# Kernel optimization log

Hardware: AMD Instinct MI355X
Metric: run time of the kernel (lower is better)

The kernel has to match this reference:

```python
import jax, jax.numpy as jnp
import numpy as np

B, S, H, NH = 4, 2048, 2048, 16
HD = H // NH
EPS = 1e-5


def setup_inputs() -> dict:
    key = jax.random.key(0)
    ks = jax.random.split(key, 5)
    return {
        "x": jax.random.normal(ks[0], (B, S, H), dtype=jnp.float32),
        "ln_w": jnp.ones((H,), dtype=jnp.float32),
        "ln_b": jnp.zeros((H,), dtype=jnp.float32),
        "c_attn_w": jax.random.normal(ks[1], (H, 3 * H), dtype=jnp.float32) * 0.02,
        "c_attn_b": jax.random.normal(ks[2], (3 * H,), dtype=jnp.float32) * 0.02,
        "c_proj_w": jax.random.normal(ks[3], (H, H), dtype=jnp.float32) * 0.02,
        "c_proj_b": jax.random.normal(ks[4], (H,), dtype=jnp.float32) * 0.02,
    }


def reference(x, ln_w, ln_b, c_attn_w, c_attn_b, c_proj_w, c_proj_b):
    residual = x
    # fused layer norm
    mu = jnp.mean(x, axis=-1, keepdims=True)
    var = jnp.mean(jnp.square(x - mu), axis=-1, keepdims=True)
    xn = (x - mu) * jax.lax.rsqrt(var + EPS) * ln_w + ln_b
    qkv = jnp.einsum("bsh,hk->bsk", xn, c_attn_w) + c_attn_b
    q, k, v = jnp.split(qkv, 3, axis=-1)
    def heads(t):
        return t.reshape(B, S, NH, HD).transpose(0, 2, 1, 3)
    q, k, v = heads(q), heads(k), heads(v)
    # causal flash attention (reference math)
    scale = 1.0 / np.sqrt(HD)
    scores = jnp.einsum("bnqd,bnkd->bnqk", q, k) * scale
    causal = jnp.tril(jnp.ones((S, S), dtype=bool))
    scores = jnp.where(causal, scores, jnp.finfo(scores.dtype).min)
    attn = jax.nn.softmax(scores, axis=-1)
    o = jnp.einsum("bnqk,bnkd->bnqd", attn, v)
    # merge heads: [B,NH,S,HD] -> [B,S,H]
    o = o.transpose(0, 2, 1, 3).reshape(B, S, H)
    # output projection + residual (fused_ffn, add_gelu=False, dropout=0)
    return jnp.einsum("bsh,hk->bsk", o, c_proj_w) + c_proj_b + residual
```

## Files before the change

kernel.cpp:

```cpp
#include <hip/hip_runtime.h>
#include <stdint.h>
#include <math.h>

#define B_  4
#define S_  2048
#define H_  2048
#define NH_ 16
#define HD_ 128
#define M_  (B_*S_)
#define N3_ (3*H_)
#define NQT_ (S_/64)
#define NT_ (H_/64)

typedef __attribute__((ext_vector_type(8))) short short8;
typedef __attribute__((ext_vector_type(4))) float floatx4;
typedef unsigned int u32;

__device__ __forceinline__ unsigned short f2bf(float f) {
  unsigned u = __float_as_uint(f);
  u += 0x7FFF + ((u >> 16) & 1);
  return (unsigned short)(u >> 16);
}

__device__ __forceinline__ void gl2lds16(const void* g, void* l) {
  __builtin_amdgcn_global_load_lds(
      (const __attribute__((address_space(1))) u32*)g,
      (__attribute__((address_space(3))) u32*)l, 16, 0, 0);
}

__global__ __launch_bounds__(256) void ln_kernel(
    const float* __restrict__ x, const float* __restrict__ w,
    const float* __restrict__ b, unsigned short* __restrict__ xn) {
  int row = blockIdx.x;
  int t = threadIdx.x;
  const float* xr = x + (size_t)row * H_;
  float4 v0 = *(const float4*)(xr + t * 4);
  float4 v1 = *(const float4*)(xr + 1024 + t * 4);
  float s  = v0.x + v0.y + v0.z + v0.w + v1.x + v1.y + v1.z + v1.w;
  float sq = v0.x*v0.x + v0.y*v0.y + v0.z*v0.z + v0.w*v0.w
           + v1.x*v1.x + v1.y*v1.y + v1.z*v1.z + v1.w*v1.w;
  #pragma unroll
  for (int m = 32; m; m >>= 1) { s += __shfl_xor(s, m); sq += __shfl_xor(sq, m); }
  __shared__ float red[8];
  int wv = t >> 6;
  if ((t & 63) == 0) { red[wv * 2] = s; red[wv * 2 + 1] = sq; }
  __syncthreads();
  s  = red[0] + red[2] + red[4] + red[6];
  sq = red[1] + red[3] + red[5] + red[7];
  float mu  = s * (1.0f / H_);
  float var = sq * (1.0f / H_) - mu * mu;
  float rs  = rsqrtf(var + 1e-5f);

  float4 w0 = *(const float4*)(w + t * 4);
  float4 b0 = *(const float4*)(b + t * 4);
  float4 w1 = *(const float4*)(w + 1024 + t * 4);
  float4 b1 = *(const float4*)(b + 1024 + t * 4);
  ushort4 o0, o1;
  o0.x = f2bf((v0.x - mu) * rs * w0.x + b0.x);
  o0.y = f2bf((v0.y - mu) * rs * w0.y + b0.y);
  o0.z = f2bf((v0.z - mu) * rs * w0.z + b0.z);
  o0.w = f2bf((v0.w - mu) * rs * w0.w + b0.w);
  o1.x = f2bf((v1.x - mu) * rs * w1.x + b1.x);
  o1.y = f2bf((v1.y - mu) * rs * w1.y + b1.y);
  o1.z = f2bf((v1.z - mu) * rs * w1.z + b1.z);
  o1.w = f2bf((v1.w - mu) * rs * w1.w + b1.w);
  unsigned short* orow = xn + (size_t)row * H_;
  *(ushort4*)(orow + t * 4) = o0;
  *(ushort4*)(orow + 1024 + t * 4) = o1;
}

__global__ __launch_bounds__(256) void transpose_f2b(
    const float* __restrict__ in, unsigned short* __restrict__ out,
    int R, int C) {
  __shared__ float tile[32][33];
  int tx = threadIdx.x & 31, ty = threadIdx.x >> 5;
  int c0 = blockIdx.x * 32, r0 = blockIdx.y * 32;
  #pragma unroll
  for (int i = 0; i < 32; i += 8)
    tile[ty + i][tx] = in[(size_t)(r0 + ty + i) * C + c0 + tx];
  __syncthreads();
  #pragma unroll
  for (int i = 0; i < 32; i += 8)
    out[(size_t)(c0 + ty + i) * R + r0 + tx] = f2bf(tile[tx][ty + i]);
}

__device__ __forceinline__ void gemm256_acc(
    const unsigned short* __restrict__ A, const unsigned short* __restrict__ Bt,
    int m0, int n0, unsigned short (*sh)[16384], floatx4 (&acc)[8][4]) {
  const int t = threadIdx.x;
  const int lane = t & 63, wv = t >> 6;
  const int l15 = lane & 15, quad = lane >> 4;
  const int wm = wv >> 2, wn = wv & 3;
  const int x7 = l15 & 7;

  const int aRB = (wm * 128 + l15) * 64;
  const int bRB = (wn * 64 + l15) * 64;
  const int kx0 = ((0 + quad) ^ x7) * 8;
  const int kx1 = ((4 + quad) ^ x7) * 8;

  const int r = t >> 3, cc = t & 7;
  const int scol = (cc ^ (r & 7)) * 8;
  const unsigned short* aSrc = A + (size_t)(m0 + r) * H_ + scol;
  const int btr = (r >> 5) * 64 + (r & 31);
  const unsigned short* bSrc = Bt + (size_t)(n0 + btr) * H_ + scol;
  const int aDst = t * 8;
  const int bDst = (r >> 5) * 4096 + (r & 31) * 64 + cc * 8;

  auto stageAll = [&](int kt, int buf) {
    const unsigned short* sa = aSrc + kt * 64;
    const unsigned short* sb = bSrc + kt * 64;
    unsigned short* da = sh[buf * 2] + aDst;
    unsigned short* db = sh[buf * 2 + 1] + bDst;
    gl2lds16(sa, da);
    gl2lds16(sa + (size_t)128 * H_, da + 8192);
    gl2lds16(sa + (size_t)64 * H_, da + 4096);
    gl2lds16(sa + (size_t)192 * H_, da + 12288);
    gl2lds16(sb, db);
    gl2lds16(sb + (size_t)128 * H_, db + 8192);
    gl2lds16(sb + (size_t)32 * H_, db + 2048);
    gl2lds16(sb + (size_t)160 * H_, db + 10240);
  };

  short8 aE[4][2], aO[4][2], b01[2][2], b23[2][2];
  auto readAE = [&](const unsigned short* Ab) {
    #pragma unroll
    for (int i = 0; i < 4; ++i) {
      aE[i][0] = *(const short8*)(Ab + aRB + i * 1024 + kx0);
      aE[i][1] = *(const short8*)(Ab + aRB + i * 1024 + kx1);
    }
  };
  auto readAO = [&](const unsigned short* Ab) {
    #pragma unroll
    for (int i = 0; i < 4; ++i) {
      aO[i][0] = *(const short8*)(Ab + aRB + (i + 4) * 1024 + kx0);
      aO[i][1] = *(const short8*)(Ab + aRB + (i + 4) * 1024 + kx1);
    }
  };
  auto readB01 = [&](const unsigned short* Bb) {
    #pragma unroll
    for (int j = 0; j < 2; ++j) {
      b01[j][0] = *(const short8*)(Bb + bRB + j * 1024 + kx0);
      b01[j][1] = *(const short8*)(Bb + bRB + j * 1024 + kx1);
    }
  };
  auto readB23 = [&](const unsigned short* Bb) {
    #pragma unroll
    for (int j = 0; j < 2; ++j) {
      b23[j][0] = *(const short8*)(Bb + bRB + (j + 2) * 1024 + kx0);
      b23[j][1] = *(const short8*)(Bb + bRB + (j + 2) * 1024 + kx1);
    }
  };

  #pragma unroll
  for (int i = 0; i < 8; i++)
    #pragma unroll
    for (int j = 0; j < 4; j++) acc[i][j] = (floatx4){0.f, 0.f, 0.f, 0.f};

  stageAll(0, 0);
  stageAll(1, 1);
  asm volatile("s_waitcnt vmcnt(8)" ::: "memory");
  __builtin_amdgcn_s_barrier();
  readAE(sh[0]); readB01(sh[1]);

  for (int n = 0; n < NT_; ++n) {
    const int buf = n & 1;
    const unsigned short* Ab = sh[buf * 2];
    const unsigned short* Bb = sh[buf * 2 + 1];

    readB23(Bb);
    asm volatile("s_waitcnt lgkmcnt(4)" ::: "memory");
    __builtin_amdgcn_sched_barrier(0);
    __builtin_amdgcn_s_setprio(1);
    #pragma unroll
    for (int i = 0; i < 4; ++i)
      #pragma unroll
      for (int j = 0; j < 2; ++j) {
        acc[i][j] = __builtin_amdgcn_mfma_f32_16x16x32_bf16(aE[i][0], b01[j][0], acc[i][j], 0, 0, 0);
        acc[i][j] = __builtin_amdgcn_mfma_f32_16x16x32_bf16(aE[i][1], b01[j][1], acc[i][j], 0, 0, 0);
      }
    __builtin_amdgcn_s_setprio(0);

    readAO(Ab);
    asm volatile("s_waitcnt lgkmcnt(8)" ::: "memory");
    __builtin_amdgcn_sched_barrier(0);
    __builtin_amdgcn_s_setprio(1);
    #pragma unroll
    for (int i = 0; i < 4; ++i)
      #pragma unroll
      for (int j = 0; j < 2; ++j) {
        acc[i][j + 2] = __builtin_amdgcn_mfma_f32_16x16x32_bf16(aE[i][0], b23[j][0], acc[i][j + 2], 0, 0, 0);
        acc[i][j + 2] = __builtin_amdgcn_mfma_f32_16x16x32_bf16(aE[i][1], b23[j][1], acc[i][j + 2], 0, 0, 0);
      }
    __builtin_amdgcn_s_setprio(0);

    asm volatile("s_waitcnt lgkmcnt(0)" ::: "memory");
    __builtin_amdgcn_sched_barrier(0);
    __builtin_amdgcn_s_setprio(1);
    #pragma unroll
    for (int i = 0; i < 4; ++i)
      #pragma unroll
      for (int j = 0; j < 2; ++j) {
        acc[i + 4][j] = __builtin_amdgcn_mfma_f32_16x16x32_bf16(aO[i][0], b01[j][0], acc[i + 4][j], 0, 0, 0);
        acc[i + 4][j] = __builtin_amdgcn_mfma_f32_16x16x32_bf16(aO[i][1], b01[j][1], acc[i + 4][j], 0, 0, 0);
      }
    __builtin_amdgcn_s_setprio(0);

    asm volatile("s_waitcnt vmcnt(0)" ::: "memory");
    __builtin_amdgcn_s_barrier();
    if (n + 1 < NT_) { readAE(sh[(buf ^ 1) * 2]); readB01(sh[(buf ^ 1) * 2 + 1]); }
    if (n + 2 < NT_) stageAll(n + 2, buf);

    __builtin_amdgcn_s_setprio(1);
    #pragma unroll
    for (int i = 0; i < 4; ++i)
      #pragma unroll
      for (int j = 0; j < 2; ++j) {
        acc[i + 4][j + 2] = __builtin_amdgcn_mfma_f32_16x16x32_bf16(aO[i][0], b23[j][0], acc[i + 4][j + 2], 0, 0, 0);
        acc[i + 4][j + 2] = __builtin_amdgcn_mfma_f32_16x16x32_bf16(aO[i][1], b23[j][1], acc[i + 4][j + 2], 0, 0, 0);
      }
    __builtin_amdgcn_s_setprio(0);
  }
}

__device__ __forceinline__ void xcd_map(int& m0, int& n0) {
  int bid = blockIdx.y * gridDim.x + blockIdx.x;
  int xcd = bid & 7, loc = bid >> 3;
  m0 = ((xcd << 2) | (loc & 3)) * 256;
  n0 = (loc >> 2) * 256;
}

__global__ __launch_bounds__(512, 2) void qkv_gemm(
    const unsigned short* __restrict__ A, const unsigned short* __restrict__ Bt,
    const float* __restrict__ bias,
    unsigned short* __restrict__ qw, unsigned short* __restrict__ kw,
    unsigned short* __restrict__ vtw) {
  __shared__ unsigned short sh[4][16384];
  int m0, n0;
  xcd_map(m0, n0);

  floatx4 acc[8][4];
  gemm256_acc(A, Bt, m0, n0, sh, acc);

  int t = threadIdx.x, lane = t & 63, wv = t >> 6;
  int l15 = lane & 15, quad = lane >> 4;
  int wm = wv >> 2, wn = wv & 3;
  int sec = n0 >> 11;
  #pragma unroll
  for (int j = 0; j < 4; ++j) {
    int nn = n0 + wn * 64 + j * 16 + l15;
    int h = (nn >> 7) & 15;
    int d = nn & 127;
    float bval = bias[nn];
    #pragma unroll
    for (int i = 0; i < 8; ++i) {
      int m = m0 + wm * 128 + i * 16 + quad * 4;
      int bb = m >> 11, s = m & 2047;
      int bh = bb * NH_ + h;
      if (sec == 2) {
        ushort4 pv;
        pv.x = f2bf(acc[i][j][0] + bval); pv.y = f2bf(acc[i][j][1] + bval);
        pv.z = f2bf(acc[i][j][2] + bval); pv.w = f2bf(acc[i][j][3] + bval);
        *(ushort4*)(vtw + ((size_t)bh * HD_ + d) * S_ + s) = pv;
      } else {
        unsigned short* dst = (sec == 0 ? qw : kw) + ((size_t)bh * S_ + s) * HD_ + d;
        #pragma unroll
        for (int reg = 0; reg < 4; reg++)
          dst[(size_t)reg * HD_] = f2bf(acc[i][j][reg] + bval);
      }
    }
  }
}

__global__ __launch_bounds__(512, 2) void proj_gemm(
    const unsigned short* __restrict__ A, const unsigned short* __restrict__ Bt,
    const float* __restrict__ bias, const float* __restrict__ resid,
    float* __restrict__ out) {
  __shared__ unsigned short sh[4][16384];
  int m0, n0;
  xcd_map(m0, n0);

  floatx4 acc[8][4];
  gemm256_acc(A, Bt, m0, n0, sh, acc);

  int t = threadIdx.x, lane = t & 63, wv = t >> 6;
  int l15 = lane & 15, quad = lane >> 4;
  int wm = wv >> 2, wn = wv & 3;
  #pragma unroll
  for (int j = 0; j < 4; ++j) {
    int nn = n0 + wn * 64 + j * 16 + l15;
    float bval = bias[nn];
    #pragma unroll
    for (int i = 0; i < 8; ++i) {
      int m = m0 + wm * 128 + i * 16 + quad * 4;
      #pragma unroll
      for (int reg = 0; reg < 4; ++reg)
        out[(size_t)(m + reg) * H_ + nn] =
            acc[i][j][reg] + bval + resid[(size_t)(m + reg) * H_ + nn];
    }
  }
}

__global__ __launch_bounds__(256) void attn_kernel(
    const unsigned short* __restrict__ qw, const unsigned short* __restrict__ kw,
    const unsigned short* __restrict__ vtw, unsigned short* __restrict__ ow) {
  __shared__ unsigned short Klds[64 * 136];
  __shared__ unsigned short Vtl[128 * 72];
  __shared__ unsigned short Pl[4][16 * 72];
  int pr = blockIdx.x, bh = blockIdx.y;
  int t = threadIdx.x, lane = t & 63, wv = t >> 6;
  int l15 = lane & 15, quad = lane >> 4;
  int h = bh & 15, bb = bh >> 4;

  const float scale = 0.08838834764831845f;
  int krr = t >> 4, kcc = (t & 15) * 8;
  int vdd = t >> 3, vss = (t & 7) * 8;
  unsigned short* plw = &Pl[wv][0];
  const unsigned short* kgb = kw + ((size_t)bh * S_ + krr) * HD_ + kcc;
  const unsigned short* vgb = vtw + ((size_t)bh * HD_ + vdd) * S_ + vss;

  short8 kreg[4], vreg[4];
  auto load_stage = [&](int kb) {
    #pragma unroll
    for (int c = 0; c < 4; c++) {
      kreg[c] = *(const short8*)(kgb + (size_t)(kb + c * 16) * HD_);
      vreg[c] = *(const short8*)(vgb + (size_t)(c * 32) * S_ + kb);
    }
  };

  #pragma unroll 1
  for (int half = 0; half < 2; half++) {
    int qt = half ? (NQT_ - 1 - pr) : pr;
    int qr = qt * 64 + wv * 16;
    int q = qr + l15;

    short8 qf[4];
    {
      const unsigned short* qbase = qw + ((size_t)bh * S_ + q) * HD_ + quad * 8;
      #pragma unroll
      for (int ks = 0; ks < 4; ks++)
        qf[ks] = *(const short8*)(qbase + ks * 32);
    }

    float m_i = -INFINITY, l_i = 0.f;
    floatx4 o[8];
    #pragma unroll
    for (int ht = 0; ht < 8; ht++) o[ht] = (floatx4){0.f, 0.f, 0.f, 0.f};

    load_stage(0);
    #pragma unroll 1
    for (int kt = 0; kt <= qt; kt++) {
      int kb = kt * 64;
      __syncthreads();
      #pragma unroll
      for (int c = 0; c < 4; c++) {
        *(short8*)(Klds + (c * 16 + krr) * 136 + kcc) = kreg[c];
        *(short8*)(Vtl + (c * 32 + vdd) * 72 + vss) = vreg[c];
      }
      __syncthreads();
      if (kt < qt) load_stage(kb + 64);

      floatx4 sv[4];
      __builtin_amdgcn_s_setprio(1);
      #pragma unroll
      for (int jm = 0; jm < 4; jm++) {
        sv[jm] = (floatx4){0.f, 0.f, 0.f, 0.f};
        #pragma unroll
        for (int ks = 0; ks < 4; ks++) {
          short8 kf = *(const short8*)(Klds + (jm * 16 + l15) * 136 + ks * 32 + quad * 8);
          sv[jm] = __builtin_amdgcn_mfma_f32_16x16x32_bf16(kf, qf[ks], sv[jm], 0, 0, 0);
        }
      }
      __builtin_amdgcn_s_setprio(0);

      float p[4][4];
      float pmax = -INFINITY;
      #pragma unroll
      for (int jm = 0; jm < 4; jm++)
        #pragma unroll
        for (int reg = 0; reg < 4; reg++) {
          float v = sv[jm][reg] * scale;
          int key = kb + jm * 16 + quad * 4 + reg;
          if (key > q) v = -1e30f;
          p[jm][reg] = v;
          pmax = fmaxf(pmax, v);
        }
      pmax = fmaxf(pmax, __shfl_xor(pmax, 16));
      pmax = fmaxf(pmax, __shfl_xor(pmax, 32));
      if (!__all(pmax - m_i <= 8.f)) {
        float mnew = fmaxf(m_i, pmax);
        float alpha = __expf(m_i - mnew);
        l_i *= alpha;
        #pragma unroll
        for (int ht = 0; ht < 8; ht++) o[ht] *= alpha;
        m_i = mnew;
      }
      float sum = 0.f;
      #pragma unroll
      for (int jm = 0; jm < 4; jm++)
        #pragma unroll
        for (int reg = 0; reg < 4; reg++) { p[jm][reg] = __expf(p[jm][reg] - m_i); sum += p[jm][reg]; }
      sum += __shfl_xor(sum, 16);
      sum += __shfl_xor(sum, 32);
      l_i += sum;

      #pragma unroll
      for (int jm = 0; jm < 4; jm++) {
        ushort4 pk;
        pk.x = f2bf(p[jm][0]); pk.y = f2bf(p[jm][1]);
        pk.z = f2bf(p[jm][2]); pk.w = f2bf(p[jm][3]);
        *(ushort4*)(plw + l15 * 72 + jm * 16 + quad * 4) = pk;
      }

      __builtin_amdgcn_s_setprio(1);
      #pragma unroll
      for (int ks2 = 0; ks2 < 2; ks2++) {
        short8 pf = *(const short8*)(plw + l15 * 72 + ks2 * 32 + quad * 8);
        #pragma unroll
        for (int ht = 0; ht < 8; ht++) {
          short8 vf = *(const short8*)(Vtl + (ht * 16 + l15) * 72 + ks2 * 32 + quad * 8);
          o[ht] = __builtin_amdgcn_mfma_f32_16x16x32_bf16(vf, pf, o[ht], 0, 0, 0);
        }
      }
      __builtin_amdgcn_s_setprio(0);
    }

    float inv = 1.0f / l_i;
    size_t base = ((size_t)(bb * S_ + q)) * H_ + h * HD_ + quad * 4;
    #pragma unroll
    for (int ht = 0; ht < 8; ht++) {
      ushort4 ov;
      ov.x = f2bf(o[ht][0] * inv); ov.y = f2bf(o[ht][1] * inv);
      ov.z = f2bf(o[ht][2] * inv); ov.w = f2bf(o[ht][3] * inv);
      *(ushort4*)(ow + base + ht * 16) = ov;
    }
  }
}

extern "C" void kernel_launch(void* const* d_in, const int* in_sizes, int n_in,
                              void* d_out, int out_size, void* d_ws, size_t ws_size,
                              hipStream_t stream) {
  (void)in_sizes; (void)n_in; (void)out_size; (void)ws_size;
  const float* x      = (const float*)d_in[0];
  const float* ln_w   = (const float*)d_in[1];
  const float* ln_b   = (const float*)d_in[2];
  const float* attn_w = (const float*)d_in[3];
  const float* attn_b = (const float*)d_in[4];
  const float* proj_w = (const float*)d_in[5];
  const float* proj_b = (const float*)d_in[6];
  float* out = (float*)d_out;

  char* ws = (char*)d_ws;
  size_t off = 0;
  auto alloc = [&](size_t bytes) {
    char* p = ws + off;
    off += (bytes + 255) & ~(size_t)255;
    return p;
  };
  unsigned short* xn     = (unsigned short*)alloc((size_t)M_ * H_ * 2);
  unsigned short* wqkvt  = (unsigned short*)alloc((size_t)N3_ * H_ * 2);
  unsigned short* wprojt = (unsigned short*)alloc((size_t)H_ * H_ * 2);
  unsigned short* qws    = (unsigned short*)alloc((size_t)M_ * H_ * 2);
  unsigned short* kws    = (unsigned short*)alloc((size_t)M_ * H_ * 2);
  unsigned short* vtws   = (unsigned short*)alloc((size_t)M_ * H_ * 2);
  unsigned short* attn_out = xn;

  ln_kernel<<<M_, 256, 0, stream>>>(x, ln_w, ln_b, xn);
  transpose_f2b<<<dim3(N3_ / 32, H_ / 32), 256, 0, stream>>>(attn_w, wqkvt, H_, N3_);
  transpose_f2b<<<dim3(H_ / 32, H_ / 32), 256, 0, stream>>>(proj_w, wprojt, H_, H_);
  qkv_gemm<<<dim3(N3_ / 256, M_ / 256), 512, 0, stream>>>(xn, wqkvt, attn_b, qws, kws, vtws);
  attn_kernel<<<dim3(NQT_ / 2, B_ * NH_), 256, 0, stream>>>(qws, kws, vtws, attn_out);
  proj_gemm<<<dim3(H_ / 256, M_ / 256), 512, 0, stream>>>(attn_out, wprojt, proj_b, x, out);
}
```

Measured before the change: 610.1 us.

## Process two 16-row query tiles per wave to reuse K/V fragments in attention

Each wave now handles 32 query rows (two 16-row MFMA tiles) instead of 16, so each K and V fragment read from LDS feeds two MFMAs, and each block covers a 128-row query span. The grid is halved to NQT/4 blocks per head, and causal pairing is done on 128-row pairs. The aim is fewer LDS reads and less K/V staging per unit of work. In exchange, register pressure roughly doubles for accumulators, which may cut occupancy, and fewer blocks with coarser causal tiles mean more masked wasted work on the diagonal.

```diff
diff --git a/kernel.cpp b/kernel.cpp
--- a/kernel.cpp
+++ b/kernel.cpp
@@ -329,26 +329,35 @@
 
   #pragma unroll 1
   for (int half = 0; half < 2; half++) {
-    int qt = half ? (NQT_ - 1 - pr) : pr;
-    int qr = qt * 64 + wv * 16;
-    int q = qr + l15;
-
-    short8 qf[4];
+    int qtLo = half ? (30 - 2 * pr) : (2 * pr);
+    int qtHi = qtLo + 1;
+    int qr = qtLo * 64 + wv * 32;
+    int q0 = qr + l15;
+    int q1 = qr + 16 + l15;
+
+    short8 qf0[4], qf1[4];
     {
-      const unsigned short* qbase = qw + ((size_t)bh * S_ + q) * HD_ + quad * 8;
-      #pragma unroll
-      for (int ks = 0; ks < 4; ks++)
-        qf[ks] = *(const short8*)(qbase + ks * 32);
-    }
-
-    float m_i = -INFINITY, l_i = 0.f;
-    floatx4 o[8];
-    #pragma unroll
-    for (int ht = 0; ht < 8; ht++) o[ht] = (floatx4){0.f, 0.f, 0.f, 0.f};
+      const unsigned short* qb0 = qw + ((size_t)bh * S_ + q0) * HD_ + quad * 8;
+      const unsigned short* qb1 = qw + ((size_t)bh * S_ + q1) * HD_ + quad * 8;
+      #pragma unroll
+      for (int ks = 0; ks < 4; ks++) {
+        qf0[ks] = *(const short8*)(qb0 + ks * 32);
+        qf1[ks] = *(const short8*)(qb1 + ks * 32);
+      }
+    }
+
+    float m_i0 = -INFINITY, l_i0 = 0.f;
+    float m_i1 = -INFINITY, l_i1 = 0.f;
+    floatx4 o0[8], o1[8];
+    #pragma unroll
+    for (int ht = 0; ht < 8; ht++) {
+      o0[ht] = (floatx4){0.f, 0.f, 0.f, 0.f};
+      o1[ht] = (floatx4){0.f, 0.f, 0.f, 0.f};
+    }
 
     load_stage(0);
     #pragma unroll 1
-    for (int kt = 0; kt <= qt; kt++) {
+    for (int kt = 0; kt <= qtHi; kt++) {
       int kb = kt * 64;
       __syncthreads();
       #pragma unroll
@@ -357,81 +366,141 @@
         *(short8*)(Vtl + (c * 32 + vdd) * 72 + vss) = vreg[c];
       }
       __syncthreads();
-      if (kt < qt) load_stage(kb + 64);
-
-      floatx4 sv[4];
+      if (kt < qtHi) load_stage(kb + 64);
+
+      floatx4 sv0[4], sv1[4];
       __builtin_amdgcn_s_setprio(1);
       #pragma unroll
       for (int jm = 0; jm < 4; jm++) {
-        sv[jm] = (floatx4){0.f, 0.f, 0.f, 0.f};
+        sv0[jm] = (floatx4){0.f, 0.f, 0.f, 0.f};
+        sv1[jm] = (floatx4){0.f, 0.f, 0.f, 0.f};
         #pragma unroll
         for (int ks = 0; ks < 4; ks++) {
           short8 kf = *(const short8*)(Klds + (jm * 16 + l15) * 136 + ks * 32 + quad * 8);
-          sv[jm] = __builtin_amdgcn_mfma_f32_16x16x32_bf16(kf, qf[ks], sv[jm], 0, 0, 0);
+          sv0[jm] = __builtin_amdgcn_mfma_f32_16x16x32_bf16(kf, qf0[ks], sv0[jm], 0, 0, 0);
+          sv1[jm] = __builtin_amdgcn_mfma_f32_16x16x32_bf16(kf, qf1[ks], sv1[jm], 0, 0, 0);
         }
       }
       __builtin_amdgcn_s_setprio(0);
 
-      float p[4][4];
-      float pmax = -INFINITY;
-      #pragma unroll
-      for (int jm = 0; jm < 4; jm++)
-        #pragma unroll
-        for (int reg = 0; reg < 4; reg++) {
-          float v = sv[jm][reg] * scale;
-          int key = kb + jm * 16 + quad * 4 + reg;
-          if (key > q) v = -1e30f;
-          p[jm][reg] = v;
-          pmax = fmaxf(pmax, v);
+      short8 pf0[2], pf1[2];
+      {
+        float p[4][4];
+        float pmax = -INFINITY;
+        #pragma unroll
+        for (int jm = 0; jm < 4; jm++)
+          #pragma unroll
+          for (int reg = 0; reg < 4; reg++) {
+            float v = sv0[jm][reg] * scale;
+            int key = kb + jm * 16 + quad * 4 + reg;
+            if (key > q0) v = -1e30f;
+            p[jm][reg] = v;
+            pmax = fmaxf(pmax, v);
+          }
+        pmax = fmaxf(pmax, __shfl_xor(pmax, 16));
+        pmax = fmaxf(pmax, __shfl_xor(pmax, 32));
+        if (!__all(pmax - m_i0 <= 8.f)) {
+          float mnew = fmaxf(m_i0, pmax);
+          float alpha = __expf(m_i0 - mnew);
+          l_i0 *= alpha;
+          #pragma unroll
+          for (int ht = 0; ht < 8; ht++) o0[ht] *= alpha;
+          m_i0 = mnew;
         }
-      pmax = fmaxf(pmax, __shfl_xor(pmax, 16));
-      pmax = fmaxf(pmax, __shfl_xor(pmax, 32));
-      if (!__all(pmax - m_i <= 8.f)) {
-        float mnew = fmaxf(m_i, pmax);
-        float alpha = __expf(m_i - mnew);
-        l_i *= alpha;
-        #pragma unroll
-        for (int ht = 0; ht < 8; ht++) o[ht] *= alpha;
-        m_i = mnew;
-      }
-      float sum = 0.f;
-      #pragma unroll
-      for (int jm = 0; jm < 4; jm++)
-        #pragma unroll
-        for (int reg = 0; reg < 4; reg++) { p[jm][reg] = __expf(p[jm][reg] - m_i); sum += p[jm][reg]; }
-      sum += __shfl_xor(sum, 16);
-      sum += __shfl_xor(sum, 32);
-      l_i += sum;
-
-      #pragma unroll
-      for (int jm = 0; jm < 4; jm++) {
-        ushort4 pk;
-        pk.x = f2bf(p[jm][0]); pk.y = f2bf(p[jm][1]);
-        pk.z = f2bf(p[jm][2]); pk.w = f2bf(p[jm][3]);
-        *(ushort4*)(plw + l15 * 72 + jm * 16 + quad * 4) = pk;
+        float sum = 0.f;
+        #pragma unroll
+        for (int jm = 0; jm < 4; jm++)
+          #pragma unroll
+          for (int reg = 0; reg < 4; reg++) { p[jm][reg] = __expf(p[jm][reg] - m_i0); sum += p[jm][reg]; }
+        sum += __shfl_xor(sum, 16);
+        sum += __shfl_xor(sum, 32);
+        l_i0 += sum;
+        #pragma unroll
+        for (int jm = 0; jm < 4; jm++) {
+          ushort4 pk;
+          pk.x = f2bf(p[jm][0]); pk.y = f2bf(p[jm][1]);
+          pk.z = f2bf(p[jm][2]); pk.w = f2bf(p[jm][3]);
+          *(ushort4*)(plw + l15 * 72 + jm * 16 + quad * 4) = pk;
+        }
+        pf0[0] = *(const short8*)(plw + l15 * 72 + quad * 8);
+        pf0[1] = *(const short8*)(plw + l15 * 72 + 32 + quad * 8);
+      }
+      {
+        float p[4][4];
+        float pmax = -INFINITY;
+        #pragma unroll
+        for (int jm = 0; jm < 4; jm++)
+          #pragma unroll
+          for (int reg = 0; reg < 4; reg++) {
+            float v = sv1[jm][reg] * scale;
+            int key = kb + jm * 16 + quad * 4 + reg;
+            if (key > q1) v = -1e30f;
+            p[jm][reg] = v;
+            pmax = fmaxf(pmax, v);
+          }
+        pmax = fmaxf(pmax, __shfl_xor(pmax, 16));
+        pmax = fmaxf(pmax, __shfl_xor(pmax, 32));
+        if (!__all(pmax - m_i1 <= 8.f)) {
+          float mnew = fmaxf(m_i1, pmax);
+          float alpha = __expf(m_i1 - mnew);
+          l_i1 *= alpha;
+          #pragma unroll
+          for (int ht = 0; ht < 8; ht++) o1[ht] *= alpha;
+          m_i1 = mnew;
+        }
+        float sum = 0.f;
+        #pragma unroll
+        for (int jm = 0; jm < 4; jm++)
+          #pragma unroll
+          for (int reg = 0; reg < 4; reg++) { p[jm][reg] = __expf(p[jm][reg] - m_i1); sum += p[jm][reg]; }
+        sum += __shfl_xor(sum, 16);
+        sum += __shfl_xor(sum, 32);
+        l_i1 += sum;
+        #pragma unroll
+        for (int jm = 0; jm < 4; jm++) {
+          ushort4 pk;
+          pk.x = f2bf(p[jm][0]); pk.y = f2bf(p[jm][1]);
+          pk.z = f2bf(p[jm][2]); pk.w = f2bf(p[jm][3]);
+          *(ushort4*)(plw + l15 * 72 + jm * 16 + quad * 4) = pk;
+        }
+        pf1[0] = *(const short8*)(plw + l15 * 72 + quad * 8);
+        pf1[1] = *(const short8*)(plw + l15 * 72 + 32 + quad * 8);
       }
 
       __builtin_amdgcn_s_setprio(1);
       #pragma unroll
       for (int ks2 = 0; ks2 < 2; ks2++) {
-        short8 pf = *(const short8*)(plw + l15 * 72 + ks2 * 32 + quad * 8);
         #pragma unroll
         for (int ht = 0; ht < 8; ht++) {
           short8 vf = *(const short8*)(Vtl + (ht * 16 + l15) * 72 + ks2 * 32 + quad * 8);
-          o[ht] = __builtin_amdgcn_mfma_f32_16x16x32_bf16(vf, pf, o[ht], 0, 0, 0);
+          o0[ht] = __builtin_amdgcn_mfma_f32_16x16x32_bf16(vf, pf0[ks2], o0[ht], 0, 0, 0);
+          o1[ht] = __builtin_amdgcn_mfma_f32_16x16x32_bf16(vf, pf1[ks2], o1[ht], 0, 0, 0);
         }
       }
       __builtin_amdgcn_s_setprio(0);
     }
 
-    float inv = 1.0f / l_i;
-    size_t base = ((size_t)(bb * S_ + q)) * H_ + h * HD_ + quad * 4;
-    #pragma unroll
-    for (int ht = 0; ht < 8; ht++) {
-      ushort4 ov;
-      ov.x = f2bf(o[ht][0] * inv); ov.y = f2bf(o[ht][1] * inv);
-      ov.z = f2bf(o[ht][2] * inv); ov.w = f2bf(o[ht][3] * inv);
-      *(ushort4*)(ow + base + ht * 16) = ov;
+    {
+      float inv = 1.0f / l_i0;
+      size_t base = ((size_t)(bb * S_ + q0)) * H_ + h * HD_ + quad * 4;
+      #pragma unroll
+      for (int ht = 0; ht < 8; ht++) {
+        ushort4 ov;
+        ov.x = f2bf(o0[ht][0] * inv); ov.y = f2bf(o0[ht][1] * inv);
+        ov.z = f2bf(o0[ht][2] * inv); ov.w = f2bf(o0[ht][3] * inv);
+        *(ushort4*)(ow + base + ht * 16) = ov;
+      }
+    }
+    {
+      float inv = 1.0f / l_i1;
+      size_t base = ((size_t)(bb * S_ + q1)) * H_ + h * HD_ + quad * 4;
+      #pragma unroll
+      for (int ht = 0; ht < 8; ht++) {
+        ushort4 ov;
+        ov.x = f2bf(o1[ht][0] * inv); ov.y = f2bf(o1[ht][1] * inv);
+        ov.z = f2bf(o1[ht][2] * inv); ov.w = f2bf(o1[ht][3] * inv);
+        *(ushort4*)(ow + base + ht * 16) = ov;
+      }
     }
   }
 }
@@ -468,6 +537,6 @@
   transpose_f2b<<<dim3(N3_ / 32, H_ / 32), 256, 0, stream>>>(attn_w, wqkvt, H_, N3_);
   transpose_f2b<<<dim3(H_ / 32, H_ / 32), 256, 0, stream>>>(proj_w, wprojt, H_, H_);
   qkv_gemm<<<dim3(N3_ / 256, M_ / 256), 512, 0, stream>>>(xn, wqkvt, attn_b, qws, kws, vtws);
-  attn_kernel<<<dim3(NQT_ / 2, B_ * NH_), 256, 0, stream>>>(qws, kws, vtws, attn_out);
+  attn_kernel<<<dim3(NQT_ / 4, B_ * NH_), 256, 0, stream>>>(qws, kws, vtws, attn_out);
   proj_gemm<<<dim3(H_ / 256, M_ / 256), 512, 0, stream>>>(attn_out, wprojt, proj_b, x, out);
 }
```

New measurement: 637.8 us. +4.5%, slower.
